# Performance work log

Hardware: AMD Instinct MI355X
Metric: run time of the kernel (lower is better)

## Reference

```python
import jax, jax.numpy as jnp
import numpy as np

THRESHOLD1 = 1.0
THRESHOLD2 = 1.0


def _conv(x, w, stride, pad):
    return jax.lax.conv_general_dilated(
        x, w, window_strides=(stride, stride),
        padding=((pad, pad), (pad, pad)),
        dimension_numbers=('NCHW', 'OIHW', 'NCHW'))


def _percentiles_1_to_99(t):
    # Faithful to torch: k = 1 + round(0.01*q*(n-1)); kthvalue = k-th smallest.
    # One sort + static gather replaces 99 kthvalue calls.
    flat = jnp.sort(t.reshape(-1))
    n = flat.shape[0]  # static under jit
    ks = np.array([1 + round(0.01 * q * (n - 1)) for q in range(1, 100)], dtype=np.int64)
    return flat[ks - 1]  # [99]


def setup_inputs() -> dict:
    key = jax.random.key(0)
    k1, k2, k3, k4 = jax.random.split(key, 4)
    x = jax.random.normal(k1, (64, 128, 56, 56), jnp.float32)
    # Kaiming-ish scaled conv weights
    w1 = jax.random.normal(k2, (256, 128, 3, 3), jnp.float32) * (2.0 / (128 * 9)) ** 0.5
    w2 = jax.random.normal(k3, (256, 256, 3, 3), jnp.float32) * (2.0 / (256 * 9)) ** 0.5
    w_id = jax.random.normal(k4, (256, 128, 1, 1), jnp.float32) * (2.0 / 128) ** 0.5
    return {"x": x, "w1": w1, "w2": w2, "w_id": w_id}


def reference(x, w1, w2, w_id):
    out1 = _conv(x, w1, 2, 1)                 # conv1: [64,256,28,28]
    a = _percentiles_1_to_99(out1)            # percentiles of UNclamped conv1 output
    out = jnp.clip(out1, 0.0, THRESHOLD1)     # out[out>t1]=t1; out[out<0]=0
    # dropout(p=0.0 / eval) is identity
    out = _conv(out, w2, 1, 1)                # conv2
    out = out + _conv(x, w_id, 2, 0)          # residual via 1x1 stride-2 downsample
    b = _percentiles_1_to_99(out)             # percentiles before second clamp
    out = jnp.clip(out, 0.0, THRESHOLD2)
    return out, a, b
```

## Files before the change

kernel.cpp:

```cpp
#include <hip/hip_runtime.h>

typedef unsigned short ushort_t;
typedef unsigned int uint_t;

using short8 = __attribute__((ext_vector_type(8))) short;
using f32x4  = __attribute__((ext_vector_type(4))) float;

#define N_BATCH   64
#define C_MID     256
#define H_OUT     28
#define W_OUT     28
#define SPATIAL   (H_OUT*W_OUT)
#define OUT_ELEMS (N_BATCH*C_MID*SPATIAL)

#define NBINS 2048
#define BIN_LO (-16.0f)
#define BIN_INV 64.0f
#define BIN_W  0.015625f

#define XT_ROW   (57*128)
#define XT_IMG   (57*57*128)
#define O1_ROW   (30*256)
#define O1_IMG   (30*30*256)

#define WAITVM(n) asm volatile("s_waitcnt vmcnt(" #n ")" ::: "memory")
#define BARRIER() asm volatile("s_barrier" ::: "memory")

__device__ __forceinline__ ushort_t f2bf(float f) {
    uint_t u = __float_as_uint(f);
    u += 0x7FFFu + ((u >> 16) & 1u);
    return (ushort_t)(u >> 16);
}

__device__ __forceinline__ void gll16(const ushort_t* g, void* l) {
    __builtin_amdgcn_global_load_lds(
        (const __attribute__((address_space(1))) unsigned int*)g,
        (__attribute__((address_space(3))) unsigned int*)l, 16, 0, 0);
}

__global__ __launch_bounds__(256) void zwtrans(
    uint_t* __restrict__ xT32, uint_t* __restrict__ o1T32,
    const float* __restrict__ w1, const float* __restrict__ w2,
    const float* __restrict__ wid, ushort_t* __restrict__ wT1,
    ushort_t* __restrict__ wT2, uint_t* __restrict__ hfA,
    uint_t* __restrict__ hfB)
{
    const int bxx = blockIdx.x, y = blockIdx.y, tid = threadIdx.x;
    if (bxx < 87) {
        int i = bxx * 256 + tid;
        int n = y;
        if (i >= 22080) return;
        if (i < 7232) {
            uint_t* base = xT32 + (size_t)n * (XT_IMG / 2);
            if (i < 3648) base[i] = 0;
            else { int j = i - 3648; int r = (j >> 6) + 1;
                   base[r * (XT_ROW / 2) + (j & 63)] = 0; }
        } else {
            int k = i - 7232;
            uint_t* base = o1T32 + (size_t)n * (O1_IMG / 2);
            if (k < 3840) base[k] = 0;
            else if (k < 7680) base[29 * (O1_ROW / 2) + (k - 3840)] = 0;
            else if (k < 11264) { int j = k - 7680; int r = (j >> 7) + 1;
                   base[r * (O1_ROW / 2) + (j & 127)] = 0; }
            else { int j = k - 11264; int r = (j >> 7) + 1;
                   base[r * (O1_ROW / 2) + 29 * 128 + (j & 127)] = 0; }
        }
    } else {
        int idx = ((bxx - 87) * 64 + y) * 256 + tid;
        if (idx < 2048)      hfA[idx] = 0;
        else if (idx < 4096) hfB[idx - 2048] = 0;
        if (idx < 256 * 1152) {
            int co = idx / 1152, k = idx % 1152;
            int g = k >> 7, ci = k & 127;
            wT1[idx] = f2bf(w1[(co * 128 + ci) * 9 + g]);
        }
        if (idx < 256 * 2432) {
            int co = idx / 2432, k = idx % 2432;
            float v;
            if (k < 2304) { int g = k >> 8, ci = k & 255; v = w2[(co * 256 + ci) * 9 + g]; }
            else          { v = wid[co * 128 + (k - 2304)]; }
            wT2[idx] = f2bf(v);
        }
    }
}

__global__ __launch_bounds__(256) void xtrans(
    const float* __restrict__ x, ushort_t* __restrict__ xT)
{
    __shared__ ushort_t t[224 * 130];
    const int tid = threadIdx.x;
    const int g = blockIdx.x, n = blockIdx.y;
    const float* xs = x + ((size_t)n * 128) * 3136 + g * 4 * 56;

    for (int it = 0; it < 112; ++it) {
        int f = it * 256 + tid;
        int ci = f / 224, rem = f % 224;
        t[rem * 130 + ci] = f2bf(xs[ci * 3136 + rem]);
    }
    __syncthreads();
    ushort_t* xo = xT + (size_t)n * XT_IMG + (g * 4 + 1) * XT_ROW + 128;
    for (int it = 0; it < 56; ++it) {
        int f = it * 256 + tid;
        int pos = f >> 6, c2 = f & 63;
        int r = pos / 56, iw = pos % 56;
        uint_t v = *(const uint_t*)&t[pos * 130 + c2 * 2];
        *(uint_t*)(xo + r * XT_ROW + iw * 128 + c2 * 2) = v;
    }
}

__global__ __launch_bounds__(256, 2) void conv1_mfma(
    const ushort_t* __restrict__ xT, const ushort_t* __restrict__ wT1,
    ushort_t* __restrict__ o1T, ushort_t* __restrict__ bh)
{
    const int bx = blockIdx.x;
    const int tid = threadIdx.x;
    const int wv = tid >> 6, lane = tid & 63;
    const int ln = lane & 15, quad = lane >> 4;
    const int n = bx / 7, rg = bx % 7, r0 = rg * 4;

    __shared__ short8 Ald[2 * 1024];
    __shared__ short8 Bp[2304];

    f32x4 acc[4][7];
    #pragma unroll
    for (int a = 0; a < 4; ++a)
        #pragma unroll
        for (int b = 0; b < 7; ++b) acc[a][b] = (f32x4){0.f, 0.f, 0.f, 0.f};

    int drb[7], cl0[7];
    #pragma unroll
    for (int b = 0; b < 7; ++b) {
        int p = b * 16 + ln;
        drb[b] = 2 * (p / 28);
        cl0[b] = p % 28;
    }

    uint_t poff[9];
    #pragma unroll
    for (int i = 0; i < 9; ++i) {
        int slot = (i * 4 + wv) * 64 + lane;
        int s2 = min(slot, 2051);
        int k8 = s2 / 513;
        int rem = s2 - k8 * 513;
        int dr = rem / 57, j = rem - dr * 57;
        int col = (j < 29) ? (2 * j) : (2 * (j - 29) + 1);
        poff[i] = (uint_t)((2 * r0 + dr) * XT_ROW + col * 128 + k8 * 8);
    }
    const uint_t aoff = (uint_t)((wv * 64 + lane) * 1152);

    const ushort_t* xTimg = xT + (size_t)n * XT_IMG;

    auto stageA = [&](int tap, int c, int buf) {
        #pragma unroll
        for (int jj = 0; jj < 4; ++jj)
            gll16(wT1 + aoff + jj * 8 + tap * 128 + c * 32,
                  (char*)Ald + buf * 16384 + (jj * 256 + wv * 64) * 16);
    };

    for (int c = 0; c < 4; ++c) {
        BARRIER();
        #pragma unroll
        for (int i = 0; i < 9; ++i)
            gll16(xTimg + poff[i] + c * 32, (char*)Bp + ((i * 4 + wv) * 64) * 16);
        if (c == 0) stageA(0, 0, 0);
        WAITVM(0);
        BARRIER();

        #pragma unroll
        for (int t = 0; t < 9; ++t) {
            const int st = c * 9 + t;
            const int buf = st & 1;
            if (t < 8)      stageA(t + 1, c, buf ^ 1);
            else if (c < 3) stageA(0, c + 1, buf ^ 1);
            if (c == 3 && t == 8) { WAITVM(0); } else { WAITVM(4); }
            const int kh = t / 3, kw = t - kh * 3;
            short8 af[4], bf[7];
            #pragma unroll
            for (int a = 0; a < 4; ++a)
                af[a] = Ald[buf * 1024 + quad * 256 + wv * 64 + a * 16 + ln];
            #pragma unroll
            for (int b = 0; b < 7; ++b) {
                int dr = drb[b] + kh;
                int j = (kw == 1) ? (29 + cl0[b]) : (cl0[b] + (kw >> 1));
                bf[b] = Bp[quad * 513 + dr * 57 + j];
            }
            __builtin_amdgcn_s_setprio(1);
            #pragma unroll
            for (int a = 0; a < 4; ++a)
                #pragma unroll
                for (int b = 0; b < 7; ++b)
                    acc[a][b] = __builtin_amdgcn_mfma_f32_16x16x32_bf16(
                        af[a], bf[b], acc[a][b], 0, 0, 0);
            __builtin_amdgcn_s_setprio(0);
        }
    }

    __syncthreads();
    uint_t* hist = (uint_t*)Ald;
    for (int i = tid; i < NBINS; i += 256) hist[i] = 0;
    __syncthreads();

    ushort_t* oimg = o1T + (size_t)n * O1_IMG;
    #pragma unroll
    for (int a = 0; a < 4; ++a) {
        int co = wv * 64 + a * 16 + quad * 4;
        #pragma unroll
        for (int b = 0; b < 7; ++b) {
            int p = b * 16 + ln;
            int h = r0 + p / 28, w = p % 28;
            ushort_t pk[4];
            #pragma unroll
            for (int r = 0; r < 4; ++r) {
                float v = acc[a][b][r];
                int bin = (int)((v - BIN_LO) * BIN_INV);
                bin = min(max(bin, 0), NBINS - 1);
                atomicAdd(&hist[bin], 1u);
                pk[r] = f2bf(fminf(fmaxf(v, 0.f), 1.f));
            }
            uint2 u; u.x = (uint_t)pk[0] | ((uint_t)pk[1] << 16);
            u.y = (uint_t)pk[2] | ((uint_t)pk[3] << 16);
            *(uint2*)(oimg + ((h + 1) * 30 + (w + 1)) * 256 + co) = u;
        }
    }

    __syncthreads();
    size_t blin = (size_t)bx * NBINS;
    for (int i = tid; i < NBINS; i += 256) bh[blin + i] = (ushort_t)hist[i];
}

__global__ __launch_bounds__(256, 2) void conv2_mfma(
    const ushort_t* __restrict__ o1T, const ushort_t* __restrict__ xT,
    const ushort_t* __restrict__ wT2, float* __restrict__ fout,
    ushort_t* __restrict__ bh)
{
    const int bx = blockIdx.x;
    const int by = blockIdx.y;
    const int tid = threadIdx.x;
    const int wv = tid >> 6, lane = tid & 63;
    const int ln = lane & 15, quad = lane >> 4;
    const int n = bx >> 2, rg = bx & 3, r0 = rg * 8;
    const int coh = wv & 1;
    const int pt  = wv >> 1;

    __shared__ short8 Ad[3 * 512];
    __shared__ short8 Bp[2 * 1280];

    f32x4 acc[4][7];
    #pragma unroll
    for (int a = 0; a < 4; ++a)
        #pragma unroll
        for (int b = 0; b < 7; ++b) acc[a][b] = (f32x4){0.f, 0.f, 0.f, 0.f};

    int prb[7], cl0[7], hlog[7];
    #pragma unroll
    for (int b = 0; b < 7; ++b) {
        int p = b * 16 + ln;
        int h = r0 + pt * 4 + p / 28;
        hlog[b] = h;
        prb[b] = (min(h, 27) - r0) * 32;
        cl0[b] = p % 28;
    }

    uint_t po[5];
    #pragma unroll
    for (int jj = 0; jj < 5; ++jj) {
        int f = (wv * 5 + jj) * 64 + lane;
        int ci8 = f / 320, rem = f % 320;
        int dr = rem >> 5, cl = rem & 31;
        po[jj] = (uint_t)(min(r0 + dr, 29) * O1_ROW + cl * 256 + ci8 * 8);
    }
    uint_t io[4];
    #pragma unroll
    for (int jj = 0; jj < 4; ++jj) {
        int i2 = min(wv * 4 + jj, 13);
        int slot = i2 * 64 + lane;
        int ci8 = slot / 224, pos = slot % 224;
        int h = min(r0 + pos / 28, 27), w = pos % 28;
        io[jj] = (uint_t)(((2 * h + 1) * 57 + (2 * w + 1)) * 128 + ci8 * 8);
    }

    const ushort_t* o1img = o1T + (size_t)n * O1_IMG;
    const ushort_t* xTimg = xT + (size_t)n * XT_IMG;
    const ushort_t* Ab0 = wT2 + (size_t)(by * 128 + lane) * 2432 + wv * 8;
    const ushort_t* Ab1 = Ab0 + (size_t)64 * 2432;

    auto stageA = [&](int k0, int buf) {
        gll16(Ab0 + k0, (char*)Ad + buf * 8192 + wv * 2048);
        gll16(Ab1 + k0, (char*)Ad + buf * 8192 + wv * 2048 + 1024);
    };
    auto stageB = [&](int hb, int coff) {
        #pragma unroll
        for (int jj = 0; jj < 5; ++jj)
            gll16(o1img + po[jj] + coff, (char*)Bp + hb * 20480 + (wv * 5 + jj) * 1024);
    };
    auto stageI = [&](int ib, int idh) {
        #pragma unroll
        for (int jj = 0; jj < 4; ++jj) {
            int i2 = min(wv * 4 + jj, 13);
            gll16(xTimg + io[jj] + idh * 32, (char*)Bp + ib * 20480 + i2 * 1024);
        }
    };

    stageB(0, 0);
    stageA(0, 0);

    for (int h = 0; h < 8; ++h) {
        #pragma unroll
        for (int t = 0; t < 9; ++t) {
            if (t < 8)      stageA((t + 1) * 256 + h * 32, (t + 1) % 3);
            else if (h < 7) stageA((h + 1) * 32, 0);
            else            stageA(2304, 0);
            if (t == 1) {
                if (h < 7) { stageB((h + 1) & 1, (h + 1) * 32); WAITVM(7); }
                else       { stageI(0, 0);                      WAITVM(6); }
            } else {
                WAITVM(2);
            }
            BARRIER();
            const int abuf = t % 3;
            const int kh = t / 3, kw = t - kh * 3;
            short8 af[4], bf[7];
            #pragma unroll
            for (int a = 0; a < 4; ++a)
                af[a] = Ad[abuf * 512 + quad * 128 + coh * 64 + a * 16 + ln];
            #pragma unroll
            for (int b = 0; b < 7; ++b)
                bf[b] = Bp[(h & 1) * 1280 + quad * 320 + prb[b] + kh * 32 + cl0[b] + kw];
            __builtin_amdgcn_s_setprio(1);
            #pragma unroll
            for (int a = 0; a < 4; ++a)
                #pragma unroll
                for (int b = 0; b < 7; ++b)
                    acc[a][b] = __builtin_amdgcn_mfma_f32_16x16x32_bf16(
                        af[a], bf[b], acc[a][b], 0, 0, 0);
            __builtin_amdgcn_s_setprio(0);
        }
    }

    #pragma unroll
    for (int idh = 0; idh < 4; ++idh) {
        if (idh < 3) { stageA(2304 + (idh + 1) * 32, (idh + 1) % 3); WAITVM(2); }
        else         { WAITVM(0); }
        BARRIER();
        if (idh < 3) stageI((idh + 1) & 1, idh + 1);
        short8 af[4], bf[7];
        #pragma unroll
        for (int a = 0; a < 4; ++a)
            af[a] = Ad[(idh % 3) * 512 + quad * 128 + coh * 64 + a * 16 + ln];
        #pragma unroll
        for (int b = 0; b < 7; ++b)
            bf[b] = Bp[(idh & 1) * 1280 + quad * 224 + pt * 112 + b * 16 + ln];
        __builtin_amdgcn_s_setprio(1);
        #pragma unroll
        for (int a = 0; a < 4; ++a)
            #pragma unroll
            for (int b = 0; b < 7; ++b)
                acc[a][b] = __builtin_amdgcn_mfma_f32_16x16x32_bf16(
                    af[a], bf[b], acc[a][b], 0, 0, 0);
        __builtin_amdgcn_s_setprio(0);
    }

    __syncthreads();
    uint_t* hist = (uint_t*)Ad;
    for (int i = tid; i < NBINS; i += 256) hist[i] = 0;
    __syncthreads();

    #pragma unroll
    for (int a = 0; a < 4; ++a) {
        int co = by * 128 + coh * 64 + a * 16 + quad * 4;
        #pragma unroll
        for (int b = 0; b < 7; ++b) {
            if (hlog[b] <= 27) {
                #pragma unroll
                for (int r = 0; r < 4; ++r) {
                    float v = acc[a][b][r];
                    int bin = (int)((v - BIN_LO) * BIN_INV);
                    bin = min(max(bin, 0), NBINS - 1);
                    atomicAdd(&hist[bin], 1u);
                    fout[((size_t)(n * 256 + co + r)) * SPATIAL +
                         hlog[b] * 28 + cl0[b]] = fminf(fmaxf(v, 0.f), 1.f);
                }
            }
        }
    }

    __syncthreads();
    size_t blin = (size_t)(by * 256 + bx) * NBINS;
    for (int i = tid; i < NBINS; i += 256) bh[blin + i] = (ushort_t)hist[i];
}

__global__ __launch_bounds__(256) void hreduce(
    const ushort_t* __restrict__ bhA, const ushort_t* __restrict__ bhB,
    uint_t* __restrict__ hfA, uint_t* __restrict__ hfB)
{
    const ushort_t* bh = blockIdx.z ? bhB : bhA;
    uint_t* hf = blockIdx.z ? hfB : hfA;
    const int nblk = blockIdx.z ? 512 : 448;
    __shared__ uint_t p[256];
    int b0 = blockIdx.x * 64;
    int binl = threadIdx.x & 63, grp = threadIdx.x >> 6;
    int rpb = (nblk + 7) / 8;
    int j0 = blockIdx.y * rpb;
    int j1 = min(j0 + rpb, nblk);
    uint_t s = 0;
    for (int j = j0 + grp; j < j1; j += 4) s += bh[(size_t)j * NBINS + b0 + binl];
    p[threadIdx.x] = s;
    __syncthreads();
    if (threadIdx.x < 64)
        atomicAdd(&hf[b0 + threadIdx.x],
                  p[threadIdx.x] + p[64 + threadIdx.x] +
                  p[128 + threadIdx.x] + p[192 + threadIdx.x]);
}

__global__ __launch_bounds__(1024) void select_k(
    const uint_t* __restrict__ hfA, const uint_t* __restrict__ hfB,
    float* __restrict__ outp)
{
    const uint_t* hf = blockIdx.x ? hfB : hfA;
    float* op = outp + blockIdx.x * 99;
    __shared__ uint_t cs[1024];
    int t = threadIdx.x;
    uint_t s = hf[2 * t] + hf[2 * t + 1];
    cs[t] = s;
    __syncthreads();
    for (int d = 1; d < 1024; d <<= 1) {
        uint_t v = (t >= d) ? cs[t - d] : 0;
        __syncthreads();
        cs[t] += v;
        __syncthreads();
    }
    if (t >= 1 && t <= 99) {
        long long k = 1 + (long long)llrint(0.01 * (double)t * (double)(OUT_ELEMS - 1));
        int lo = 0, hi = 1023;
        while (lo < hi) { int mid = (lo + hi) >> 1; if ((long long)cs[mid] < k) lo = mid + 1; else hi = mid; }
        long long cum = (lo == 0) ? 0 : (long long)cs[lo - 1];
        int b = lo * 2;
        while (cum + (long long)hf[b] < k) { cum += hf[b]; ++b; }
        op[t - 1] = BIN_LO + ((float)b + 0.5f) * BIN_W;
    }
}

extern "C" void kernel_launch(void* const* d_in, const int* in_sizes, int n_in,
                              void* d_out, int out_size, void* d_ws, size_t ws_size,
                              hipStream_t stream)
{
    const float* x   = (const float*)d_in[0];
    const float* w1  = (const float*)d_in[1];
    const float* w2  = (const float*)d_in[2];
    const float* wid = (const float*)d_in[3];
    float* out = (float*)d_out;

    char* ws = (char*)d_ws;
    ushort_t* xT  = (ushort_t*)ws;
    ushort_t* o1T = (ushort_t*)(ws + 53235712);
    ushort_t* wT1 = (ushort_t*)(ws + 82731008);
    ushort_t* wT2 = (ushort_t*)(ws + 83320832);
    ushort_t* bhA = (ushort_t*)(ws + 84566016);
    ushort_t* bhB = (ushort_t*)(ws + 86401024);
    uint_t*   hfA = (uint_t*)  (ws + 88498176);
    uint_t*   hfB = (uint_t*)  (ws + 88506368);

    zwtrans<<<dim3(125, 64), 256, 0, stream>>>((uint_t*)xT, (uint_t*)o1T,
                                               w1, w2, wid, wT1, wT2, hfA, hfB);
    xtrans<<<dim3(14, 64), 256, 0, stream>>>(x, xT);

    conv1_mfma<<<448, 256, 0, stream>>>(xT, wT1, o1T, bhA);
    conv2_mfma<<<dim3(256, 2), 256, 0, stream>>>(o1T, xT, wT2, out, bhB);

    hreduce<<<dim3(32, 8, 2), 256, 0, stream>>>(bhA, bhB, hfA, hfB);
    select_k<<<2, 1024, 0, stream>>>(hfA, hfB, out + OUT_ELEMS);
}
```

Baseline: 354.7 us.

## Retile conv2 to full 256-channel blocks over 4-row strips and vectorize xtrans loads

conv2 now has each block compute all 256 output channels for a 4-row strip (448 blocks instead of 512 blocks with 128 channels over 8 rows). Each wave owns 64 channels and the A operand is double-buffered. The B tile is loaded once per channel chunk and its load is no longer overlapped, since it sits behind a full wait and barrier. The change removes the padded, wasted rows (8 rows covering 28 meant the last group did extra work) and halves duplicate activation loads, but exposes the B-tile load latency. xtrans also switches to float4 global reads.

```diff
diff --git a/kernel.cpp b/kernel.cpp
--- a/kernel.cpp
+++ b/kernel.cpp
@@ -92,10 +92,15 @@
     const int g = blockIdx.x, n = blockIdx.y;
     const float* xs = x + ((size_t)n * 128) * 3136 + g * 4 * 56;
 
-    for (int it = 0; it < 112; ++it) {
+    #pragma unroll
+    for (int it = 0; it < 28; ++it) {
         int f = it * 256 + tid;
-        int ci = f / 224, rem = f % 224;
-        t[rem * 130 + ci] = f2bf(xs[ci * 3136 + rem]);
+        int ci = f / 56, r4 = f % 56;
+        float4 v = *(const float4*)(xs + ci * 3136 + r4 * 4);
+        t[(r4 * 4 + 0) * 130 + ci] = f2bf(v.x);
+        t[(r4 * 4 + 1) * 130 + ci] = f2bf(v.y);
+        t[(r4 * 4 + 2) * 130 + ci] = f2bf(v.z);
+        t[(r4 * 4 + 3) * 130 + ci] = f2bf(v.w);
     }
     __syncthreads();
     ushort_t* xo = xT + (size_t)n * XT_IMG + (g * 4 + 1) * XT_ROW + 128;
@@ -234,16 +239,13 @@
     ushort_t* __restrict__ bh)
 {
     const int bx = blockIdx.x;
-    const int by = blockIdx.y;
     const int tid = threadIdx.x;
     const int wv = tid >> 6, lane = tid & 63;
     const int ln = lane & 15, quad = lane >> 4;
-    const int n = bx >> 2, rg = bx & 3, r0 = rg * 8;
-    const int coh = wv & 1;
-    const int pt  = wv >> 1;
-
-    __shared__ short8 Ad[3 * 512];
-    __shared__ short8 Bp[2 * 1280];
+    const int n = bx / 7, rg = bx % 7, r0 = rg * 4;
+
+    __shared__ short8 Ald[2 * 1024];
+    __shared__ short8 Bp[768];
 
     f32x4 acc[4][7];
     #pragma unroll
@@ -251,81 +253,77 @@
         #pragma unroll
         for (int b = 0; b < 7; ++b) acc[a][b] = (f32x4){0.f, 0.f, 0.f, 0.f};
 
-    int prb[7], cl0[7], hlog[7];
+    int rwb[7], cl0[7];
     #pragma unroll
     for (int b = 0; b < 7; ++b) {
         int p = b * 16 + ln;
-        int h = r0 + pt * 4 + p / 28;
-        hlog[b] = h;
-        prb[b] = (min(h, 27) - r0) * 32;
+        rwb[b] = (p / 28) * 32;
         cl0[b] = p % 28;
     }
 
-    uint_t po[5];
-    #pragma unroll
-    for (int jj = 0; jj < 5; ++jj) {
-        int f = (wv * 5 + jj) * 64 + lane;
-        int ci8 = f / 320, rem = f % 320;
+    uint_t po[3];
+    #pragma unroll
+    for (int jj = 0; jj < 3; ++jj) {
+        int f = (wv * 3 + jj) * 64 + lane;
+        int ci8 = f / 192, rem = f % 192;
         int dr = rem >> 5, cl = rem & 31;
-        po[jj] = (uint_t)(min(r0 + dr, 29) * O1_ROW + cl * 256 + ci8 * 8);
-    }
-    uint_t io[4];
-    #pragma unroll
-    for (int jj = 0; jj < 4; ++jj) {
-        int i2 = min(wv * 4 + jj, 13);
+        po[jj] = (uint_t)((r0 + dr) * O1_ROW + cl * 256 + ci8 * 8);
+    }
+    uint_t io[2];
+    int isl[2];
+    #pragma unroll
+    for (int jj = 0; jj < 2; ++jj) {
+        int i2 = min(wv * 2 + jj, 6);
+        isl[jj] = i2;
         int slot = i2 * 64 + lane;
-        int ci8 = slot / 224, pos = slot % 224;
-        int h = min(r0 + pos / 28, 27), w = pos % 28;
+        int ci8 = slot / 112, pos = slot % 112;
+        int h = r0 + pos / 28, w = pos % 28;
         io[jj] = (uint_t)(((2 * h + 1) * 57 + (2 * w + 1)) * 128 + ci8 * 8);
     }
+    const ushort_t* asrc = wT2 + (size_t)(wv * 64 + lane) * 2432;
 
     const ushort_t* o1img = o1T + (size_t)n * O1_IMG;
     const ushort_t* xTimg = xT + (size_t)n * XT_IMG;
-    const ushort_t* Ab0 = wT2 + (size_t)(by * 128 + lane) * 2432 + wv * 8;
-    const ushort_t* Ab1 = Ab0 + (size_t)64 * 2432;
 
     auto stageA = [&](int k0, int buf) {
-        gll16(Ab0 + k0, (char*)Ad + buf * 8192 + wv * 2048);
-        gll16(Ab1 + k0, (char*)Ad + buf * 8192 + wv * 2048 + 1024);
+        #pragma unroll
+        for (int jj = 0; jj < 4; ++jj)
+            gll16(asrc + k0 + jj * 8,
+                  (char*)Ald + buf * 16384 + (jj * 256 + wv * 64) * 16);
     };
-    auto stageB = [&](int hb, int coff) {
-        #pragma unroll
-        for (int jj = 0; jj < 5; ++jj)
-            gll16(o1img + po[jj] + coff, (char*)Bp + hb * 20480 + (wv * 5 + jj) * 1024);
+    auto stageB = [&](int coff) {
+        #pragma unroll
+        for (int jj = 0; jj < 3; ++jj)
+            gll16(o1img + po[jj] + coff, (char*)Bp + (wv * 3 + jj) * 1024);
     };
-    auto stageI = [&](int ib, int idh) {
-        #pragma unroll
-        for (int jj = 0; jj < 4; ++jj) {
-            int i2 = min(wv * 4 + jj, 13);
-            gll16(xTimg + io[jj] + idh * 32, (char*)Bp + ib * 20480 + i2 * 1024);
-        }
+    auto stageI = [&](int idh) {
+        #pragma unroll
+        for (int jj = 0; jj < 2; ++jj)
+            gll16(xTimg + io[jj] + idh * 32, (char*)Bp + isl[jj] * 1024);
     };
 
-    stageB(0, 0);
-    stageA(0, 0);
-
-    for (int h = 0; h < 8; ++h) {
+    for (int c = 0; c < 8; ++c) {
+        BARRIER();
+        stageB(c * 32);
+        if (c == 0) stageA(0, 0);
+        WAITVM(0);
+        BARRIER();
+
         #pragma unroll
         for (int t = 0; t < 9; ++t) {
-            if (t < 8)      stageA((t + 1) * 256 + h * 32, (t + 1) % 3);
-            else if (h < 7) stageA((h + 1) * 32, 0);
-            else            stageA(2304, 0);
-            if (t == 1) {
-                if (h < 7) { stageB((h + 1) & 1, (h + 1) * 32); WAITVM(7); }
-                else       { stageI(0, 0);                      WAITVM(6); }
-            } else {
-                WAITVM(2);
-            }
-            BARRIER();
-            const int abuf = t % 3;
+            const int st = c * 9 + t;
+            const int buf = st & 1;
+            if (t < 8)      stageA((t + 1) * 256 + c * 32, buf ^ 1);
+            else if (c < 7) stageA(c * 32 + 32, buf ^ 1);
+            if (c == 7 && t == 8) { WAITVM(0); } else { WAITVM(4); }
             const int kh = t / 3, kw = t - kh * 3;
             short8 af[4], bf[7];
             #pragma unroll
             for (int a = 0; a < 4; ++a)
-                af[a] = Ad[abuf * 512 + quad * 128 + coh * 64 + a * 16 + ln];
+                af[a] = Ald[buf * 1024 + quad * 256 + wv * 64 + a * 16 + ln];
             #pragma unroll
             for (int b = 0; b < 7; ++b)
-                bf[b] = Bp[(h & 1) * 1280 + quad * 320 + prb[b] + kh * 32 + cl0[b] + kw];
+                bf[b] = Bp[quad * 192 + rwb[b] + kh * 32 + cl0[b] + kw];
             __builtin_amdgcn_s_setprio(1);
             #pragma unroll
             for (int a = 0; a < 4; ++a)
@@ -339,17 +337,19 @@
 
     #pragma unroll
     for (int idh = 0; idh < 4; ++idh) {
-        if (idh < 3) { stageA(2304 + (idh + 1) * 32, (idh + 1) % 3); WAITVM(2); }
-        else         { WAITVM(0); }
-        BARRIER();
-        if (idh < 3) stageI((idh + 1) & 1, idh + 1);
+        BARRIER();
+        stageI(idh);
+        if (idh == 0) stageA(2304, 0);
+        WAITVM(0);
+        BARRIER();
+        if (idh < 3) stageA(2304 + (idh + 1) * 32, (idh + 1) & 1);
         short8 af[4], bf[7];
         #pragma unroll
         for (int a = 0; a < 4; ++a)
-            af[a] = Ad[(idh % 3) * 512 + quad * 128 + coh * 64 + a * 16 + ln];
+            af[a] = Ald[(idh & 1) * 1024 + quad * 256 + wv * 64 + a * 16 + ln];
         #pragma unroll
         for (int b = 0; b < 7; ++b)
-            bf[b] = Bp[(idh & 1) * 1280 + quad * 224 + pt * 112 + b * 16 + ln];
+            bf[b] = Bp[quad * 112 + b * 16 + ln];
         __builtin_amdgcn_s_setprio(1);
         #pragma unroll
         for (int a = 0; a < 4; ++a)
@@ -361,31 +361,31 @@
     }
 
     __syncthreads();
-    uint_t* hist = (uint_t*)Ad;
+    uint_t* hist = (uint_t*)Ald;
     for (int i = tid; i < NBINS; i += 256) hist[i] = 0;
     __syncthreads();
 
     #pragma unroll
     for (int a = 0; a < 4; ++a) {
-        int co = by * 128 + coh * 64 + a * 16 + quad * 4;
+        int co = wv * 64 + a * 16 + quad * 4;
         #pragma unroll
         for (int b = 0; b < 7; ++b) {
-            if (hlog[b] <= 27) {
-                #pragma unroll
-                for (int r = 0; r < 4; ++r) {
-                    float v = acc[a][b][r];
-                    int bin = (int)((v - BIN_LO) * BIN_INV);
-                    bin = min(max(bin, 0), NBINS - 1);
-                    atomicAdd(&hist[bin], 1u);
-                    fout[((size_t)(n * 256 + co + r)) * SPATIAL +
-                         hlog[b] * 28 + cl0[b]] = fminf(fmaxf(v, 0.f), 1.f);
-                }
+            int p = b * 16 + ln;
+            int h = r0 + p / 28, w = p % 28;
+            #pragma unroll
+            for (int r = 0; r < 4; ++r) {
+                float v = acc[a][b][r];
+                int bin = (int)((v - BIN_LO) * BIN_INV);
+                bin = min(max(bin, 0), NBINS - 1);
+                atomicAdd(&hist[bin], 1u);
+                fout[((size_t)(n * 256 + co + r)) * SPATIAL +
+                     h * 28 + w] = fminf(fmaxf(v, 0.f), 1.f);
             }
         }
     }
 
     __syncthreads();
-    size_t blin = (size_t)(by * 256 + bx) * NBINS;
+    size_t blin = (size_t)bx * NBINS;
     for (int i = tid; i < NBINS; i += 256) bh[blin + i] = (ushort_t)hist[i];
 }
 
@@ -395,7 +395,7 @@
 {
     const ushort_t* bh = blockIdx.z ? bhB : bhA;
     uint_t* hf = blockIdx.z ? hfB : hfA;
-    const int nblk = blockIdx.z ? 512 : 448;
+    const int nblk = 448;
     __shared__ uint_t p[256];
     int b0 = blockIdx.x * 64;
     int binl = threadIdx.x & 63, grp = threadIdx.x >> 6;
@@ -465,7 +465,7 @@
     xtrans<<<dim3(14, 64), 256, 0, stream>>>(x, xT);
 
     conv1_mfma<<<448, 256, 0, stream>>>(xT, wT1, o1T, bhA);
-    conv2_mfma<<<dim3(256, 2), 256, 0, stream>>>(o1T, xT, wT2, out, bhB);
+    conv2_mfma<<<448, 256, 0, stream>>>(o1T, xT, wT2, out, bhB);
 
     hreduce<<<dim3(32, 8, 2), 256, 0, stream>>>(bhA, bhB, hfA, hfB);
     select_k<<<2, 1024, 0, stream>>>(hfA, hfB, out + OUT_ELEMS);
```

Result: no change. 358.3 us (+1.0%).

## Merge per-block histograms with global atomics and vectorize xtrans loads

Applied to the files above, without the earlier changes.

Each conv kernel now adds its shared-memory histogram straight into the global histogram with atomics, skipping zero bins. This removes the per-block ushort histogram buffers and the separate hreduce launch. The xtrans kernel also reads x as float4 and unrolls its loop, which cuts the number of global load instructions. In exchange there is global atomic contention at the end of every conv block, and the wider shared-memory scatter may cause more bank conflicts.

```diff
diff --git a/kernel.cpp b/kernel.cpp
--- a/kernel.cpp
+++ b/kernel.cpp
@@ -92,10 +92,15 @@
     const int g = blockIdx.x, n = blockIdx.y;
     const float* xs = x + ((size_t)n * 128) * 3136 + g * 4 * 56;
 
-    for (int it = 0; it < 112; ++it) {
+    #pragma unroll
+    for (int it = 0; it < 28; ++it) {
         int f = it * 256 + tid;
-        int ci = f / 224, rem = f % 224;
-        t[rem * 130 + ci] = f2bf(xs[ci * 3136 + rem]);
+        int ci = f / 56, r4 = f % 56;
+        float4 v = *(const float4*)(xs + ci * 3136 + r4 * 4);
+        t[(r4 * 4 + 0) * 130 + ci] = f2bf(v.x);
+        t[(r4 * 4 + 1) * 130 + ci] = f2bf(v.y);
+        t[(r4 * 4 + 2) * 130 + ci] = f2bf(v.z);
+        t[(r4 * 4 + 3) * 130 + ci] = f2bf(v.w);
     }
     __syncthreads();
     ushort_t* xo = xT + (size_t)n * XT_IMG + (g * 4 + 1) * XT_ROW + 128;
@@ -110,7 +115,7 @@
 
 __global__ __launch_bounds__(256, 2) void conv1_mfma(
     const ushort_t* __restrict__ xT, const ushort_t* __restrict__ wT1,
-    ushort_t* __restrict__ o1T, ushort_t* __restrict__ bh)
+    ushort_t* __restrict__ o1T, uint_t* __restrict__ hf)
 {
     const int bx = blockIdx.x;
     const int tid = threadIdx.x;
@@ -224,14 +229,16 @@
     }
 
     __syncthreads();
-    size_t blin = (size_t)bx * NBINS;
-    for (int i = tid; i < NBINS; i += 256) bh[blin + i] = (ushort_t)hist[i];
+    for (int i = tid; i < NBINS; i += 256) {
+        uint_t v = hist[i];
+        if (v) atomicAdd(&hf[i], v);
+    }
 }
 
 __global__ __launch_bounds__(256, 2) void conv2_mfma(
     const ushort_t* __restrict__ o1T, const ushort_t* __restrict__ xT,
     const ushort_t* __restrict__ wT2, float* __restrict__ fout,
-    ushort_t* __restrict__ bh)
+    uint_t* __restrict__ hf)
 {
     const int bx = blockIdx.x;
     const int by = blockIdx.y;
@@ -385,31 +392,10 @@
     }
 
     __syncthreads();
-    size_t blin = (size_t)(by * 256 + bx) * NBINS;
-    for (int i = tid; i < NBINS; i += 256) bh[blin + i] = (ushort_t)hist[i];
-}
-
-__global__ __launch_bounds__(256) void hreduce(
-    const ushort_t* __restrict__ bhA, const ushort_t* __restrict__ bhB,
-    uint_t* __restrict__ hfA, uint_t* __restrict__ hfB)
-{
-    const ushort_t* bh = blockIdx.z ? bhB : bhA;
-    uint_t* hf = blockIdx.z ? hfB : hfA;
-    const int nblk = blockIdx.z ? 512 : 448;
-    __shared__ uint_t p[256];
-    int b0 = blockIdx.x * 64;
-    int binl = threadIdx.x & 63, grp = threadIdx.x >> 6;
-    int rpb = (nblk + 7) / 8;
-    int j0 = blockIdx.y * rpb;
-    int j1 = min(j0 + rpb, nblk);
-    uint_t s = 0;
-    for (int j = j0 + grp; j < j1; j += 4) s += bh[(size_t)j * NBINS + b0 + binl];
-    p[threadIdx.x] = s;
-    __syncthreads();
-    if (threadIdx.x < 64)
-        atomicAdd(&hf[b0 + threadIdx.x],
-                  p[threadIdx.x] + p[64 + threadIdx.x] +
-                  p[128 + threadIdx.x] + p[192 + threadIdx.x]);
+    for (int i = tid; i < NBINS; i += 256) {
+        uint_t v = hist[i];
+        if (v) atomicAdd(&hf[i], v);
+    }
 }
 
 __global__ __launch_bounds__(1024) void select_k(
@@ -455,8 +441,6 @@
     ushort_t* o1T = (ushort_t*)(ws + 53235712);
     ushort_t* wT1 = (ushort_t*)(ws + 82731008);
     ushort_t* wT2 = (ushort_t*)(ws + 83320832);
-    ushort_t* bhA = (ushort_t*)(ws + 84566016);
-    ushort_t* bhB = (ushort_t*)(ws + 86401024);
     uint_t*   hfA = (uint_t*)  (ws + 88498176);
     uint_t*   hfB = (uint_t*)  (ws + 88506368);
 
@@ -464,9 +448,8 @@
                                                w1, w2, wid, wT1, wT2, hfA, hfB);
     xtrans<<<dim3(14, 64), 256, 0, stream>>>(x, xT);
 
-    conv1_mfma<<<448, 256, 0, stream>>>(xT, wT1, o1T, bhA);
-    conv2_mfma<<<dim3(256, 2), 256, 0, stream>>>(o1T, xT, wT2, out, bhB);
-
-    hreduce<<<dim3(32, 8, 2), 256, 0, stream>>>(bhA, bhB, hfA, hfB);
+    conv1_mfma<<<448, 256, 0, stream>>>(xT, wT1, o1T, hfA);
+    conv2_mfma<<<dim3(256, 2), 256, 0, stream>>>(o1T, xT, wT2, out, hfB);
+
     select_k<<<2, 1024, 0, stream>>>(hfA, hfB, out + OUT_ELEMS);
 }
```

After: 340.3 us. -4.1%, faster.
